# Optimization experiments

Measured on AMD Instinct MI355X. Metric: run time of the kernel, lower is better.

The kernel has to match this reference:

```python
import jax, jax.numpy as jnp
import numpy as np

IN_FEATURES = 256
OUT_FEATURES = 64
ALPHA = 0.2  # leaky relu slope


def _xavier_uniform(key, shape, gain=1.414):
    fan_in, fan_out = shape[0], shape[1]
    limit = gain * np.sqrt(6.0 / (fan_in + fan_out))
    return jax.random.uniform(key, shape, jnp.float32, -limit, limit)


def setup_inputs() -> dict:
    key = jax.random.key(0)
    k_h, k_W, k_a = jax.random.split(key, 3)
    h = jax.random.normal(k_h, (8, 2048, IN_FEATURES), dtype=jnp.float32)
    W = _xavier_uniform(k_W, (IN_FEATURES, OUT_FEATURES))
    a = _xavier_uniform(k_a, (2 * OUT_FEATURES, 1))
    return {"h": h, "W": W, "a": a}


def reference(h, W, a):
    # h: [B, N, F_in], W: [F_in, D], a: [2D, 1]
    Wh = h @ W  # [B, N, D]
    D = Wh.shape[-1]
    a1 = a[:D, 0]   # attends to source node i (repeat_interleave side)
    a2 = a[D:, 0]   # attends to target node j (repeat side)
    f1 = Wh @ a1    # [B, N]
    f2 = Wh @ a2    # [B, N]
    # e[b, i, j] = leakyrelu(a1.Wh[b,i] + a2.Wh[b,j])  -- identical math to
    # the original's O(N^2 * 2D) repeat/concat, without materializing it.
    e = jax.nn.leaky_relu(f1[:, :, None] + f2[:, None, :], negative_slope=ALPHA)  # [B, N, N]
    # NOTE: original applies softmax over dim=1 (over i, per column j).
    attention = jax.nn.softmax(e, axis=1)  # [B, N, N]
    # dropout is identity in eval mode
    h_prime = jnp.einsum('bij,bjd->bid', attention, Wh)  # [B, N, D]
    return jax.nn.elu(h_prime)  # concat=True path
```

## Files before the change

### kernel.cpp

```cpp
#include <hip/hip_runtime.h>

#define B 8
#define N 2048
#define KF 256
#define DF 64
#define LOG2E 1.44269504088896340736f
#define IC 8
#define ICH (N / IC)

typedef __attribute__((ext_vector_type(8))) short short8;
typedef __attribute__((ext_vector_type(4))) float float4v;

__device__ __forceinline__ float fexp2(float x) {
#if __has_builtin(__builtin_amdgcn_exp2f)
    return __builtin_amdgcn_exp2f(x);
#else
    return exp2f(x);
#endif
}
__device__ __forceinline__ float flog2(float x) {
#if __has_builtin(__builtin_amdgcn_logf)
    return __builtin_amdgcn_logf(x);
#else
    return log2f(x);
#endif
}
__device__ __forceinline__ float eluf(float x) {
    return x > 0.f ? x : fexp2(x * LOG2E) - 1.0f;
}
__device__ __forceinline__ short bf16r(float x) {
    unsigned u = __float_as_uint(x);
    return (short)((u + 0x8000u) >> 16);
}

__global__ __launch_bounds__(256) void k_v(const float* __restrict__ W,
                                           const float* __restrict__ a,
                                           short* __restrict__ WTg,
                                           float* __restrict__ v12) {
    int t = threadIdx.x;
    if (blockIdx.x < 64) {
        int idx = blockIdx.x * 256 + t;
        int k = idx >> 6, n = idx & 63;
        WTg[n * KF + k] = bf16r(W[idx]);
    } else {
        float s1 = 0.f, s2 = 0.f;
        for (int d = 0; d < DF; d++) {
            float w = W[t * DF + d];
            s1 = fmaf(w, a[d], s1);
            s2 = fmaf(w, a[DF + d], s2);
        }
        v12[t] = s1;
        v12[KF + t] = s2;
    }
}

__global__ __launch_bounds__(256) void k_wh(const float* __restrict__ h,
                                            const short* __restrict__ WTg,
                                            const float* __restrict__ v12,
                                            short* __restrict__ WhT,
                                            float* __restrict__ f1,
                                            float* __restrict__ f2) {
    __shared__ float lred[4 * 16 * DF];
    __shared__ float lp[2][4][16];
    int t = threadIdx.x;
    int wv = t >> 6, lane = t & 63;
    int n15 = lane & 15, q = lane >> 4;
    long i0 = (long)blockIdx.x * 16;
    const float* hr = h + (i0 + n15) * KF + wv * 64;
    const short* bp0 = WTg + n15 * KF + wv * 64;

    float4v acc0 = {0.f, 0.f, 0.f, 0.f}, acc1 = acc0, acc2 = acc0, acc3 = acc0;
    float p1 = 0.f, p2 = 0.f;

    #pragma unroll
    for (int s = 0; s < 2; s++) {
        int k0 = s * 32 + q * 8;
        int kg = wv * 64 + k0;
        float4 a0 = *(const float4*)(hr + k0);
        float4 a1 = *(const float4*)(hr + k0 + 4);
        float4 u0 = *(const float4*)(v12 + kg);
        float4 u1 = *(const float4*)(v12 + kg + 4);
        float4 x0 = *(const float4*)(v12 + KF + kg);
        float4 x1 = *(const float4*)(v12 + KF + kg + 4);
        p1 = fmaf(a0.x, u0.x, fmaf(a0.y, u0.y, fmaf(a0.z, u0.z, fmaf(a0.w, u0.w, p1))));
        p1 = fmaf(a1.x, u1.x, fmaf(a1.y, u1.y, fmaf(a1.z, u1.z, fmaf(a1.w, u1.w, p1))));
        p2 = fmaf(a0.x, x0.x, fmaf(a0.y, x0.y, fmaf(a0.z, x0.z, fmaf(a0.w, x0.w, p2))));
        p2 = fmaf(a1.x, x1.x, fmaf(a1.y, x1.y, fmaf(a1.z, x1.z, fmaf(a1.w, x1.w, p2))));

        short8 af = { bf16r(a0.x), bf16r(a0.y), bf16r(a0.z), bf16r(a0.w),
                      bf16r(a1.x), bf16r(a1.y), bf16r(a1.z), bf16r(a1.w) };
        const short* bp = bp0 + k0;
        short8 b0 = *(const short8*)(bp);
        short8 b1 = *(const short8*)(bp + 16 * KF);
        short8 b2 = *(const short8*)(bp + 32 * KF);
        short8 b3 = *(const short8*)(bp + 48 * KF);

        acc0 = __builtin_amdgcn_mfma_f32_16x16x32_bf16(af, b0, acc0, 0, 0, 0);
        acc1 = __builtin_amdgcn_mfma_f32_16x16x32_bf16(af, b1, acc1, 0, 0, 0);
        acc2 = __builtin_amdgcn_mfma_f32_16x16x32_bf16(af, b2, acc2, 0, 0, 0);
        acc3 = __builtin_amdgcn_mfma_f32_16x16x32_bf16(af, b3, acc3, 0, 0, 0);
    }

    #define STASH(nb, A)                                                 \
        {                                                                \
            _Pragma("unroll")                                            \
            for (int r = 0; r < 4; r++)                                  \
                lred[wv * 1024 + (q * 4 + r) * DF + nb * 16 + n15] = A[r]; \
        }
    STASH(0, acc0) STASH(1, acc1) STASH(2, acc2) STASH(3, acc3)
    #undef STASH

    p1 += __shfl_xor(p1, 16, 64); p1 += __shfl_xor(p1, 32, 64);
    p2 += __shfl_xor(p2, 16, 64); p2 += __shfl_xor(p2, 32, 64);
    if (q == 0) { lp[0][wv][n15] = p1; lp[1][wv][n15] = p2; }
    __syncthreads();

    int d = t & 63, ig = t >> 6;
    int bb = (int)(i0 >> 11);
    int il = (int)(i0 & (N - 1));
    float s0 = 0.f, s1 = 0.f, s2 = 0.f, s3 = 0.f;
    #pragma unroll
    for (int w = 0; w < 4; w++) {
        const float* lr = lred + w * 1024 + (ig * 4) * DF + d;
        s0 += lr[0]; s1 += lr[DF]; s2 += lr[2 * DF]; s3 += lr[3 * DF];
    }
    short4 pk = make_short4(bf16r(s0), bf16r(s1), bf16r(s2), bf16r(s3));
    int jj = il + ig * 4;
    *(short4*)(WhT + (((long)bb * 8 + (jj >> 8)) * 64 + d) * 256 + (jj & 255)) = pk;

    if (t < 16) {
        float v = lp[0][0][t] + lp[0][1][t] + lp[0][2][t] + lp[0][3][t];
        f1[i0 + t] = v;
    } else if (t < 32) {
        int tt = t - 16;
        float v = lp[1][0][tt] + lp[1][1][tt] + lp[1][2][tt] + lp[1][3][tt];
        f2[i0 + tt] = v;
    }
}

__global__ __launch_bounds__(256) void k_denom(const float* __restrict__ f1,
                                               const float* __restrict__ f2,
                                               float* __restrict__ dpart) {
    __shared__ float lf1[ICH];
    int t = threadIdx.x;
    int b = blockIdx.z, ic = blockIdx.y;
    int j = blockIdx.x * 256 + t;
    lf1[t] = f1[b * N + ic * ICH + t];
    __syncthreads();
    float f2j = f2[b * N + j];
    float s = 0.f;
    for (int ii = 0; ii < ICH; ii++) {
        float e = (lf1[ii] + f2j) * LOG2E;
        s += fexp2(fmaxf(e, 0.2f * e));
    }
    dpart[((long)ic * B + b) * N + j] = s;
}

__global__ __launch_bounds__(256) void k_attn(const short* __restrict__ WhT,
                                              const float* __restrict__ f1,
                                              const float* __restrict__ f2,
                                              const float* __restrict__ dpart,
                                              float* __restrict__ out) {
    __shared__ uint4 ls[64][33];
    __shared__ float2 lc[2][256];
    int t = threadIdx.x;
    int wv = t >> 6, lane = t & 63;
    int n15 = lane & 15, q = lane >> 4;
    int it = blockIdx.x, b = blockIdx.y;
    int i0 = it * 64 + wv * 16;

    float f1L = f1[b * N + i0 + n15] * LOG2E;
    const uint4* wsrc = (const uint4*)WhT + (long)b * 8 * 2048;
    const float* f2b = f2 + b * N;
    const float* dpb = dpart + b * N;

    uint4 r0, r1, r2, r3, r4, r5, r6, r7;
    float pf2, pd0, pd1, pd2, pd3, pd4, pd5, pd6, pd7;

    #define LOADC(cc) {                                     \
        const uint4* gp = wsrc + (cc) * 2048;               \
        r0 = gp[t];        r1 = gp[256 + t];                \
        r2 = gp[512 + t];  r3 = gp[768 + t];                \
        r4 = gp[1024 + t]; r5 = gp[1280 + t];               \
        r6 = gp[1536 + t]; r7 = gp[1792 + t];               \
    }
    #define LOADP(cc) {                                     \
        int jb = (cc) * 256 + t;                            \
        pf2 = f2b[jb];                                      \
        pd0 = dpb[jb];               pd1 = dpb[16384 + jb]; \
        pd2 = dpb[2 * 16384 + jb];   pd3 = dpb[3 * 16384 + jb]; \
        pd4 = dpb[4 * 16384 + jb];   pd5 = dpb[5 * 16384 + jb]; \
        pd6 = dpb[6 * 16384 + jb];   pd7 = dpb[7 * 16384 + jb]; \
    }
    #define STOREC() {                                      \
        int rb = t >> 5, cl = t & 31;                       \
        ls[rb][cl] = r0;      ls[8 + rb][cl] = r1;          \
        ls[16 + rb][cl] = r2; ls[24 + rb][cl] = r3;         \
        ls[32 + rb][cl] = r4; ls[40 + rb][cl] = r5;         \
        ls[48 + rb][cl] = r6; ls[56 + rb][cl] = r7;         \
    }
    #define LCC(buf) {                                      \
        float den = ((pd0 + pd1) + (pd2 + pd3)) + ((pd4 + pd5) + (pd6 + pd7)); \
        lc[buf][t] = make_float2(pf2 * LOG2E, -flog2(den)); \
    }

    LOADC(0) LOADP(0)
    STOREC() LCC(0)
    __syncthreads();

    float4v acc0 = {0.f, 0.f, 0.f, 0.f}, acc1 = acc0, acc2 = acc0, acc3 = acc0;

    for (int c = 0; c < 8; c++) {
        int cur = c & 1;
        if (c < 7) { LOADC(c + 1) LOADP(c + 1) }

        const short* lsS = (const short*)&ls[0][0];
        const float4* lcf = (const float4*)&lc[cur][0];
        #pragma unroll
        for (int js = 0; js < 8; js++) {
            const float4* cp4 = lcf + js * 16 + q * 4;
            float4 p01 = cp4[0], p23 = cp4[1], p45 = cp4[2], p67 = cp4[3];
            short8 af;
            #define PENT(F2L, LS2, DI)                        \
                {                                             \
                    float t0 = f1L + (F2L);                   \
                    float l2 = fmaxf(t0, 0.2f * t0);          \
                    af[DI] = bf16r(fexp2(l2 + (LS2)));        \
                }
            PENT(p01.x, p01.y, 0) PENT(p01.z, p01.w, 1)
            PENT(p23.x, p23.y, 2) PENT(p23.z, p23.w, 3)
            PENT(p45.x, p45.y, 4) PENT(p45.z, p45.w, 5)
            PENT(p67.x, p67.y, 6) PENT(p67.z, p67.w, 7)
            #undef PENT

            const short* bp = lsS + js * 32 + q * 8;
            short8 b0 = *(const short8*)(bp + (n15 +  0) * 264);
            short8 b1 = *(const short8*)(bp + (n15 + 16) * 264);
            short8 b2 = *(const short8*)(bp + (n15 + 32) * 264);
            short8 b3 = *(const short8*)(bp + (n15 + 48) * 264);

            acc0 = __builtin_amdgcn_mfma_f32_16x16x32_bf16(af, b0, acc0, 0, 0, 0);
            acc1 = __builtin_amdgcn_mfma_f32_16x16x32_bf16(af, b1, acc1, 0, 0, 0);
            acc2 = __builtin_amdgcn_mfma_f32_16x16x32_bf16(af, b2, acc2, 0, 0, 0);
            acc3 = __builtin_amdgcn_mfma_f32_16x16x32_bf16(af, b3, acc3, 0, 0, 0);
        }

        if (c < 7) {
            __syncthreads();
            STOREC() LCC((c + 1) & 1)
            __syncthreads();
        }
    }
    #undef LOADC
    #undef LOADP
    #undef STOREC
    #undef LCC

    float* ob = out + ((long)b * N + i0 + q * 4) * DF + n15;
    #pragma unroll
    for (int r = 0; r < 4; r++) {
        ob[r * DF + 0]  = eluf(acc0[r]);
        ob[r * DF + 16] = eluf(acc1[r]);
        ob[r * DF + 32] = eluf(acc2[r]);
        ob[r * DF + 48] = eluf(acc3[r]);
    }
}

extern "C" void kernel_launch(void* const* d_in, const int* in_sizes, int n_in,
                              void* d_out, int out_size, void* d_ws, size_t ws_size,
                              hipStream_t stream) {
    const float* h = (const float*)d_in[0];
    const float* W = (const float*)d_in[1];
    const float* a = (const float*)d_in[2];
    float* out = (float*)d_out;

    char* ws = (char*)d_ws;
    const size_t NB = (size_t)B * N;
    size_t off = 0;
    short* WTg   = (short*)(ws + off); off += (size_t)KF * DF * sizeof(short);
    float* v12   = (float*)(ws + off); off += 2 * KF * sizeof(float);
    short* WhT   = (short*)(ws + off); off += NB * DF * sizeof(short);
    float* f1    = (float*)(ws + off); off += NB * sizeof(float);
    float* f2    = (float*)(ws + off); off += NB * sizeof(float);
    float* dpart = (float*)(ws + off); off += (size_t)IC * NB * sizeof(float);
    (void)off; (void)ws_size;

    k_v<<<65, 256, 0, stream>>>(W, a, WTg, v12);
    k_wh<<<NB / 16, 256, 0, stream>>>(h, WTg, v12, WhT, f1, f2);
    k_denom<<<dim3(N / 256, IC, B), 256, 0, stream>>>(f1, f2, dpart);
    k_attn<<<dim3(N / 64, B), 256, 0, stream>>>(WhT, f1, f2, dpart, out);
}
```

Before: 105.1 us.

## Fuse all four stages into one cooperative kernel with grid syncs

Replaces four separate launches with a single cooperative kernel of 256 blocks that uses grid-wide syncs between the weight prep, Wh projection, denominator and attention stages. Each block now handles 64 rows in the projection stage and 512 i-values in the denominator stage, so the denominator partials drop from 8 to 4 chunks. This removes launch gaps and inter-kernel drain, in exchange for less parallelism per stage (256 blocks) and the cost of the grid barriers.

```diff
diff --git a/kernel.cpp b/kernel.cpp
--- a/kernel.cpp
+++ b/kernel.cpp
@@ -1,12 +1,13 @@
 #include <hip/hip_runtime.h>
+#include <hip/hip_cooperative_groups.h>
+
+namespace cg = cooperative_groups;
 
 #define B 8
 #define N 2048
 #define KF 256
 #define DF 64
 #define LOG2E 1.44269504088896340736f
-#define IC 8
-#define ICH (N / IC)
 
 typedef __attribute__((ext_vector_type(8))) short short8;
 typedef __attribute__((ext_vector_type(4))) float float4v;
@@ -32,17 +33,27 @@
     unsigned u = __float_as_uint(x);
     return (short)((u + 0x8000u) >> 16);
 }
-
-__global__ __launch_bounds__(256) void k_v(const float* __restrict__ W,
-                                           const float* __restrict__ a,
-                                           short* __restrict__ WTg,
-                                           float* __restrict__ v12) {
+#define DOT4(c, u, p) \
+    p = fmaf(c.x, u.x, fmaf(c.y, u.y, fmaf(c.z, u.z, fmaf(c.w, u.w, p))));
+
+__global__ __launch_bounds__(256) void k_mega(
+    const float* __restrict__ h, const float* __restrict__ W,
+    const float* __restrict__ a, short* __restrict__ WTg,
+    float* __restrict__ v12, short* __restrict__ WhT,
+    float* __restrict__ f1, float* __restrict__ f2,
+    float* __restrict__ dpart, float* __restrict__ out) {
+    __shared__ __align__(16) unsigned char smem[37888];
+    cg::grid_group grid = cg::this_grid();
     int t = threadIdx.x;
-    if (blockIdx.x < 64) {
-        int idx = blockIdx.x * 256 + t;
+    int bx = blockIdx.x;
+    int wv = t >> 6, lane = t & 63;
+    int n15 = lane & 15, q = lane >> 4;
+
+    if (bx < 64) {
+        int idx = bx * 256 + t;
         int k = idx >> 6, n = idx & 63;
         WTg[n * KF + k] = bf16r(W[idx]);
-    } else {
+    } else if (bx == 64) {
         float s1 = 0.f, s2 = 0.f;
         for (int d = 0; d < DF; d++) {
             float w = W[t * DF + d];
@@ -52,217 +63,219 @@
         v12[t] = s1;
         v12[KF + t] = s2;
     }
-}
-
-__global__ __launch_bounds__(256) void k_wh(const float* __restrict__ h,
-                                            const short* __restrict__ WTg,
-                                            const float* __restrict__ v12,
-                                            short* __restrict__ WhT,
-                                            float* __restrict__ f1,
-                                            float* __restrict__ f2) {
-    __shared__ float lred[4 * 16 * DF];
-    __shared__ float lp[2][4][16];
-    int t = threadIdx.x;
-    int wv = t >> 6, lane = t & 63;
-    int n15 = lane & 15, q = lane >> 4;
-    long i0 = (long)blockIdx.x * 16;
-    const float* hr = h + (i0 + n15) * KF + wv * 64;
-    const short* bp0 = WTg + n15 * KF + wv * 64;
-
-    float4v acc0 = {0.f, 0.f, 0.f, 0.f}, acc1 = acc0, acc2 = acc0, acc3 = acc0;
-    float p1 = 0.f, p2 = 0.f;
-
-    #pragma unroll
-    for (int s = 0; s < 2; s++) {
-        int k0 = s * 32 + q * 8;
-        int kg = wv * 64 + k0;
-        float4 a0 = *(const float4*)(hr + k0);
-        float4 a1 = *(const float4*)(hr + k0 + 4);
-        float4 u0 = *(const float4*)(v12 + kg);
-        float4 u1 = *(const float4*)(v12 + kg + 4);
-        float4 x0 = *(const float4*)(v12 + KF + kg);
-        float4 x1 = *(const float4*)(v12 + KF + kg + 4);
-        p1 = fmaf(a0.x, u0.x, fmaf(a0.y, u0.y, fmaf(a0.z, u0.z, fmaf(a0.w, u0.w, p1))));
-        p1 = fmaf(a1.x, u1.x, fmaf(a1.y, u1.y, fmaf(a1.z, u1.z, fmaf(a1.w, u1.w, p1))));
-        p2 = fmaf(a0.x, x0.x, fmaf(a0.y, x0.y, fmaf(a0.z, x0.z, fmaf(a0.w, x0.w, p2))));
-        p2 = fmaf(a1.x, x1.x, fmaf(a1.y, x1.y, fmaf(a1.z, x1.z, fmaf(a1.w, x1.w, p2))));
-
-        short8 af = { bf16r(a0.x), bf16r(a0.y), bf16r(a0.z), bf16r(a0.w),
-                      bf16r(a1.x), bf16r(a1.y), bf16r(a1.z), bf16r(a1.w) };
-        const short* bp = bp0 + k0;
-        short8 b0 = *(const short8*)(bp);
-        short8 b1 = *(const short8*)(bp + 16 * KF);
-        short8 b2 = *(const short8*)(bp + 32 * KF);
-        short8 b3 = *(const short8*)(bp + 48 * KF);
-
-        acc0 = __builtin_amdgcn_mfma_f32_16x16x32_bf16(af, b0, acc0, 0, 0, 0);
-        acc1 = __builtin_amdgcn_mfma_f32_16x16x32_bf16(af, b1, acc1, 0, 0, 0);
-        acc2 = __builtin_amdgcn_mfma_f32_16x16x32_bf16(af, b2, acc2, 0, 0, 0);
-        acc3 = __builtin_amdgcn_mfma_f32_16x16x32_bf16(af, b3, acc3, 0, 0, 0);
+    grid.sync();
+
+    {
+        float* lred = (float*)smem;
+        float* lp = (float*)(smem + 16384);
+        const short* bq = WTg + n15 * KF + wv * 64 + q * 8;
+        short8 s0b0 = *(const short8*)(bq);
+        short8 s0b1 = *(const short8*)(bq + 16 * KF);
+        short8 s0b2 = *(const short8*)(bq + 32 * KF);
+        short8 s0b3 = *(const short8*)(bq + 48 * KF);
+        short8 s1b0 = *(const short8*)(bq + 32);
+        short8 s1b1 = *(const short8*)(bq + 16 * KF + 32);
+        short8 s1b2 = *(const short8*)(bq + 32 * KF + 32);
+        short8 s1b3 = *(const short8*)(bq + 48 * KF + 32);
+        const float* vv = v12 + wv * 64 + q * 8;
+        float4 u00 = *(const float4*)(vv);
+        float4 u01 = *(const float4*)(vv + 4);
+        float4 u10 = *(const float4*)(vv + 32);
+        float4 u11 = *(const float4*)(vv + 36);
+        float4 x00 = *(const float4*)(vv + KF);
+        float4 x01 = *(const float4*)(vv + KF + 4);
+        float4 x10 = *(const float4*)(vv + KF + 32);
+        float4 x11 = *(const float4*)(vv + KF + 36);
+
+        const float* hr = h + ((long)bx * 64 + n15) * KF + wv * 64 + q * 8;
+        float4 c0 = *(const float4*)(hr);
+        float4 c1 = *(const float4*)(hr + 4);
+        float4 c2 = *(const float4*)(hr + 32);
+        float4 c3 = *(const float4*)(hr + 36);
+
+        #pragma unroll
+        for (int rt = 0; rt < 4; rt++) {
+            float4 m0, m1, m2, m3;
+            if (rt < 3) {
+                const float* hn = hr + (rt + 1) * 16 * KF;
+                m0 = *(const float4*)(hn);
+                m1 = *(const float4*)(hn + 4);
+                m2 = *(const float4*)(hn + 32);
+                m3 = *(const float4*)(hn + 36);
+            }
+            float p1 = 0.f, p2 = 0.f;
+            DOT4(c0, u00, p1) DOT4(c1, u01, p1) DOT4(c2, u10, p1) DOT4(c3, u11, p1)
+            DOT4(c0, x00, p2) DOT4(c1, x01, p2) DOT4(c2, x10, p2) DOT4(c3, x11, p2)
+
+            short8 af0 = { bf16r(c0.x), bf16r(c0.y), bf16r(c0.z), bf16r(c0.w),
+                           bf16r(c1.x), bf16r(c1.y), bf16r(c1.z), bf16r(c1.w) };
+            short8 af1 = { bf16r(c2.x), bf16r(c2.y), bf16r(c2.z), bf16r(c2.w),
+                           bf16r(c3.x), bf16r(c3.y), bf16r(c3.z), bf16r(c3.w) };
+            float4v acc0 = {0.f, 0.f, 0.f, 0.f}, acc1 = acc0, acc2 = acc0, acc3 = acc0;
+            acc0 = __builtin_amdgcn_mfma_f32_16x16x32_bf16(af0, s0b0, acc0, 0, 0, 0);
+            acc0 = __builtin_amdgcn_mfma_f32_16x16x32_bf16(af1, s1b0, acc0, 0, 0, 0);
+            acc1 = __builtin_amdgcn_mfma_f32_16x16x32_bf16(af0, s0b1, acc1, 0, 0, 0);
+            acc1 = __builtin_amdgcn_mfma_f32_16x16x32_bf16(af1, s1b1, acc1, 0, 0, 0);
+            acc2 = __builtin_amdgcn_mfma_f32_16x16x32_bf16(af0, s0b2, acc2, 0, 0, 0);
+            acc2 = __builtin_amdgcn_mfma_f32_16x16x32_bf16(af1, s1b2, acc2, 0, 0, 0);
+            acc3 = __builtin_amdgcn_mfma_f32_16x16x32_bf16(af0, s0b3, acc3, 0, 0, 0);
+            acc3 = __builtin_amdgcn_mfma_f32_16x16x32_bf16(af1, s1b3, acc3, 0, 0, 0);
+
+            #define STASH(nb, A)                                                 \
+                {                                                                \
+                    _Pragma("unroll")                                            \
+                    for (int r = 0; r < 4; r++)                                  \
+                        lred[wv * 1024 + (q * 4 + r) * DF + nb * 16 + n15] = A[r]; \
+                }
+            STASH(0, acc0) STASH(1, acc1) STASH(2, acc2) STASH(3, acc3)
+            #undef STASH
+            p1 += __shfl_xor(p1, 16, 64); p1 += __shfl_xor(p1, 32, 64);
+            p2 += __shfl_xor(p2, 16, 64); p2 += __shfl_xor(p2, 32, 64);
+            if (q == 0) { lp[wv * 16 + n15] = p1; lp[64 + wv * 16 + n15] = p2; }
+            __syncthreads();
+
+            long i0 = (long)bx * 64 + rt * 16;
+            int d = t & 63, ig = t >> 6;
+            int bb = (int)(i0 >> 11);
+            int il = (int)(i0 & (N - 1));
+            float s0 = 0.f, s1 = 0.f, s2 = 0.f, s3 = 0.f;
+            #pragma unroll
+            for (int w = 0; w < 4; w++) {
+                const float* lr = lred + w * 1024 + (ig * 4) * DF + d;
+                s0 += lr[0]; s1 += lr[DF]; s2 += lr[2 * DF]; s3 += lr[3 * DF];
+            }
+            short4 pk = make_short4(bf16r(s0), bf16r(s1), bf16r(s2), bf16r(s3));
+            int jj = il + ig * 4;
+            *(short4*)(WhT + (((long)bb * 8 + (jj >> 8)) * 64 + d) * 256 + (jj & 255)) = pk;
+
+            if (t < 16) {
+                f1[i0 + t] = lp[t] + lp[16 + t] + lp[32 + t] + lp[48 + t];
+            } else if (t < 32) {
+                int tt = t + 48;
+                f2[i0 + t - 16] = lp[tt] + lp[16 + tt] + lp[32 + tt] + lp[48 + tt];
+            }
+            __syncthreads();
+            c0 = m0; c1 = m1; c2 = m2; c3 = m3;
+        }
     }
-
-    #define STASH(nb, A)                                                 \
-        {                                                                \
-            _Pragma("unroll")                                            \
-            for (int r = 0; r < 4; r++)                                  \
-                lred[wv * 1024 + (q * 4 + r) * DF + nb * 16 + n15] = A[r]; \
-        }
-    STASH(0, acc0) STASH(1, acc1) STASH(2, acc2) STASH(3, acc3)
-    #undef STASH
-
-    p1 += __shfl_xor(p1, 16, 64); p1 += __shfl_xor(p1, 32, 64);
-    p2 += __shfl_xor(p2, 16, 64); p2 += __shfl_xor(p2, 32, 64);
-    if (q == 0) { lp[0][wv][n15] = p1; lp[1][wv][n15] = p2; }
-    __syncthreads();
-
-    int d = t & 63, ig = t >> 6;
-    int bb = (int)(i0 >> 11);
-    int il = (int)(i0 & (N - 1));
-    float s0 = 0.f, s1 = 0.f, s2 = 0.f, s3 = 0.f;
-    #pragma unroll
-    for (int w = 0; w < 4; w++) {
-        const float* lr = lred + w * 1024 + (ig * 4) * DF + d;
-        s0 += lr[0]; s1 += lr[DF]; s2 += lr[2 * DF]; s3 += lr[3 * DF];
+    grid.sync();
+
+    {
+        float* lf1 = (float*)smem;
+        int jb = bx & 7, ic = (bx >> 3) & 3, b2 = bx >> 5;
+        lf1[t] = f1[b2 * N + ic * 512 + t];
+        lf1[256 + t] = f1[b2 * N + ic * 512 + 256 + t];
+        __syncthreads();
+        float f2j = f2[b2 * N + jb * 256 + t];
+        float s = 0.f;
+        for (int ii = 0; ii < 512; ii++) {
+            float e = (lf1[ii] + f2j) * LOG2E;
+            s += fexp2(fmaxf(e, 0.2f * e));
+        }
+        dpart[((long)ic * B + b2) * N + jb * 256 + t] = s;
+        __syncthreads();
     }
-    short4 pk = make_short4(bf16r(s0), bf16r(s1), bf16r(s2), bf16r(s3));
-    int jj = il + ig * 4;
-    *(short4*)(WhT + (((long)bb * 8 + (jj >> 8)) * 64 + d) * 256 + (jj & 255)) = pk;
-
-    if (t < 16) {
-        float v = lp[0][0][t] + lp[0][1][t] + lp[0][2][t] + lp[0][3][t];
-        f1[i0 + t] = v;
-    } else if (t < 32) {
-        int tt = t - 16;
-        float v = lp[1][0][tt] + lp[1][1][tt] + lp[1][2][tt] + lp[1][3][tt];
-        f2[i0 + tt] = v;
-    }
-}
-
-__global__ __launch_bounds__(256) void k_denom(const float* __restrict__ f1,
-                                               const float* __restrict__ f2,
-                                               float* __restrict__ dpart) {
-    __shared__ float lf1[ICH];
-    int t = threadIdx.x;
-    int b = blockIdx.z, ic = blockIdx.y;
-    int j = blockIdx.x * 256 + t;
-    lf1[t] = f1[b * N + ic * ICH + t];
-    __syncthreads();
-    float f2j = f2[b * N + j];
-    float s = 0.f;
-    for (int ii = 0; ii < ICH; ii++) {
-        float e = (lf1[ii] + f2j) * LOG2E;
-        s += fexp2(fmaxf(e, 0.2f * e));
-    }
-    dpart[((long)ic * B + b) * N + j] = s;
-}
-
-__global__ __launch_bounds__(256) void k_attn(const short* __restrict__ WhT,
-                                              const float* __restrict__ f1,
-                                              const float* __restrict__ f2,
-                                              const float* __restrict__ dpart,
-                                              float* __restrict__ out) {
-    __shared__ uint4 ls[64][33];
-    __shared__ float2 lc[2][256];
-    int t = threadIdx.x;
-    int wv = t >> 6, lane = t & 63;
-    int n15 = lane & 15, q = lane >> 4;
-    int it = blockIdx.x, b = blockIdx.y;
-    int i0 = it * 64 + wv * 16;
-
-    float f1L = f1[b * N + i0 + n15] * LOG2E;
-    const uint4* wsrc = (const uint4*)WhT + (long)b * 8 * 2048;
-    const float* f2b = f2 + b * N;
-    const float* dpb = dpart + b * N;
-
-    uint4 r0, r1, r2, r3, r4, r5, r6, r7;
-    float pf2, pd0, pd1, pd2, pd3, pd4, pd5, pd6, pd7;
-
-    #define LOADC(cc) {                                     \
-        const uint4* gp = wsrc + (cc) * 2048;               \
-        r0 = gp[t];        r1 = gp[256 + t];                \
-        r2 = gp[512 + t];  r3 = gp[768 + t];                \
-        r4 = gp[1024 + t]; r5 = gp[1280 + t];               \
-        r6 = gp[1536 + t]; r7 = gp[1792 + t];               \
-    }
-    #define LOADP(cc) {                                     \
-        int jb = (cc) * 256 + t;                            \
-        pf2 = f2b[jb];                                      \
-        pd0 = dpb[jb];               pd1 = dpb[16384 + jb]; \
-        pd2 = dpb[2 * 16384 + jb];   pd3 = dpb[3 * 16384 + jb]; \
-        pd4 = dpb[4 * 16384 + jb];   pd5 = dpb[5 * 16384 + jb]; \
-        pd6 = dpb[6 * 16384 + jb];   pd7 = dpb[7 * 16384 + jb]; \
-    }
-    #define STOREC() {                                      \
-        int rb = t >> 5, cl = t & 31;                       \
-        ls[rb][cl] = r0;      ls[8 + rb][cl] = r1;          \
-        ls[16 + rb][cl] = r2; ls[24 + rb][cl] = r3;         \
-        ls[32 + rb][cl] = r4; ls[40 + rb][cl] = r5;         \
-        ls[48 + rb][cl] = r6; ls[56 + rb][cl] = r7;         \
-    }
-    #define LCC(buf) {                                      \
-        float den = ((pd0 + pd1) + (pd2 + pd3)) + ((pd4 + pd5) + (pd6 + pd7)); \
-        lc[buf][t] = make_float2(pf2 * LOG2E, -flog2(den)); \
-    }
-
-    LOADC(0) LOADP(0)
-    STOREC() LCC(0)
-    __syncthreads();
-
-    float4v acc0 = {0.f, 0.f, 0.f, 0.f}, acc1 = acc0, acc2 = acc0, acc3 = acc0;
-
-    for (int c = 0; c < 8; c++) {
-        int cur = c & 1;
-        if (c < 7) { LOADC(c + 1) LOADP(c + 1) }
-
-        const short* lsS = (const short*)&ls[0][0];
-        const float4* lcf = (const float4*)&lc[cur][0];
+    grid.sync();
+
+    {
+        uint4 (*ls)[33] = (uint4 (*)[33])smem;
+        float2 (*lc)[256] = (float2 (*)[256])(smem + 33792);
+        int it = bx & 31, b3 = bx >> 5;
+        int i0 = it * 64 + wv * 16;
+
+        float f1L = f1[b3 * N + i0 + n15] * LOG2E;
+        const uint4* wsrc = (const uint4*)WhT + (long)b3 * 8 * 2048;
+        const float* f2b = f2 + b3 * N;
+        const float* dpb = dpart + b3 * N;
+
+        uint4 r0, r1, r2, r3, r4, r5, r6, r7;
+        float pf2, pd0, pd1, pd2, pd3;
+
+        #define LOADC(cc) {                                     \
+            const uint4* gp = wsrc + (cc) * 2048;               \
+            r0 = gp[t];        r1 = gp[256 + t];                \
+            r2 = gp[512 + t];  r3 = gp[768 + t];                \
+            r4 = gp[1024 + t]; r5 = gp[1280 + t];               \
+            r6 = gp[1536 + t]; r7 = gp[1792 + t];               \
+        }
+        #define LOADP(cc) {                                     \
+            int jb2 = (cc) * 256 + t;                           \
+            pf2 = f2b[jb2];                                     \
+            pd0 = dpb[jb2];              pd1 = dpb[16384 + jb2];\
+            pd2 = dpb[2 * 16384 + jb2];  pd3 = dpb[3 * 16384 + jb2]; \
+        }
+        #define STOREC() {                                      \
+            int rb = t >> 5, cl = t & 31;                       \
+            ls[rb][cl] = r0;      ls[8 + rb][cl] = r1;          \
+            ls[16 + rb][cl] = r2; ls[24 + rb][cl] = r3;         \
+            ls[32 + rb][cl] = r4; ls[40 + rb][cl] = r5;         \
+            ls[48 + rb][cl] = r6; ls[56 + rb][cl] = r7;         \
+        }
+        #define LCC(buf) {                                      \
+            float den = (pd0 + pd1) + (pd2 + pd3);              \
+            lc[buf][t] = make_float2(pf2 * LOG2E, -flog2(den)); \
+        }
+
+        LOADC(0) LOADP(0)
+        STOREC() LCC(0)
+        __syncthreads();
+
+        float4v acc0 = {0.f, 0.f, 0.f, 0.f}, acc1 = acc0, acc2 = acc0, acc3 = acc0;
+
+        for (int c = 0; c < 8; c++) {
+            int cur = c & 1;
+            if (c < 7) { LOADC(c + 1) LOADP(c + 1) }
+
+            const short* lsS = (const short*)smem;
+            const float4* lcf = (const float4*)&lc[cur][0];
+            #pragma unroll
+            for (int js = 0; js < 8; js++) {
+                const float4* cp4 = lcf + js * 16 + q * 4;
+                float4 p01 = cp4[0], p23 = cp4[1], p45 = cp4[2], p67 = cp4[3];
+                short8 af;
+                #define PENT(F2L, LS2, DI)                        \
+                    {                                             \
+                        float t0 = f1L + (F2L);                   \
+                        float l2 = fmaxf(t0, 0.2f * t0);          \
+                        af[DI] = bf16r(fexp2(l2 + (LS2)));        \
+                    }
+                PENT(p01.x, p01.y, 0) PENT(p01.z, p01.w, 1)
+                PENT(p23.x, p23.y, 2) PENT(p23.z, p23.w, 3)
+                PENT(p45.x, p45.y, 4) PENT(p45.z, p45.w, 5)
+                PENT(p67.x, p67.y, 6) PENT(p67.z, p67.w, 7)
+                #undef PENT
+
+                const short* bp = lsS + js * 32 + q * 8;
+                short8 b0 = *(const short8*)(bp + (n15 +  0) * 264);
+                short8 b1 = *(const short8*)(bp + (n15 + 16) * 264);
+                short8 b2 = *(const short8*)(bp + (n15 + 32) * 264);
+                short8 b3 = *(const short8*)(bp + (n15 + 48) * 264);
+
+                acc0 = __builtin_amdgcn_mfma_f32_16x16x32_bf16(af, b0, acc0, 0, 0, 0);
+                acc1 = __builtin_amdgcn_mfma_f32_16x16x32_bf16(af, b1, acc1, 0, 0, 0);
+                acc2 = __builtin_amdgcn_mfma_f32_16x16x32_bf16(af, b2, acc2, 0, 0, 0);
+                acc3 = __builtin_amdgcn_mfma_f32_16x16x32_bf16(af, b3, acc3, 0, 0, 0);
+            }
+
+            if (c < 7) {
+                __syncthreads();
+                STOREC() LCC((c + 1) & 1)
+                __syncthreads();
+            }
+        }
+        #undef LOADC
+        #undef LOADP
+        #undef STOREC
+        #undef LCC
+
+        float* ob = out + ((long)b3 * N + i0 + q * 4) * DF + n15;
         #pragma unroll
-        for (int js = 0; js < 8; js++) {
-            const float4* cp4 = lcf + js * 16 + q * 4;
-            float4 p01 = cp4[0], p23 = cp4[1], p45 = cp4[2], p67 = cp4[3];
-            short8 af;
-            #define PENT(F2L, LS2, DI)                        \
-                {                                             \
-                    float t0 = f1L + (F2L);                   \
-                    float l2 = fmaxf(t0, 0.2f * t0);          \
-                    af[DI] = bf16r(fexp2(l2 + (LS2)));        \
-                }
-            PENT(p01.x, p01.y, 0) PENT(p01.z, p01.w, 1)
-            PENT(p23.x, p23.y, 2) PENT(p23.z, p23.w, 3)
-            PENT(p45.x, p45.y, 4) PENT(p45.z, p45.w, 5)
-            PENT(p67.x, p67.y, 6) PENT(p67.z, p67.w, 7)
-            #undef PENT
-
-            const short* bp = lsS + js * 32 + q * 8;
-            short8 b0 = *(const short8*)(bp + (n15 +  0) * 264);
-            short8 b1 = *(const short8*)(bp + (n15 + 16) * 264);
-            short8 b2 = *(const short8*)(bp + (n15 + 32) * 264);
-            short8 b3 = *(const short8*)(bp + (n15 + 48) * 264);
-
-            acc0 = __builtin_amdgcn_mfma_f32_16x16x32_bf16(af, b0, acc0, 0, 0, 0);
-            acc1 = __builtin_amdgcn_mfma_f32_16x16x32_bf16(af, b1, acc1, 0, 0, 0);
-            acc2 = __builtin_amdgcn_mfma_f32_16x16x32_bf16(af, b2, acc2, 0, 0, 0);
-            acc3 = __builtin_amdgcn_mfma_f32_16x16x32_bf16(af, b3, acc3, 0, 0, 0);
-        }
-
-        if (c < 7) {
-            __syncthreads();
-            STOREC() LCC((c + 1) & 1)
-            __syncthreads();
-        }
-    }
-    #undef LOADC
-    #undef LOADP
-    #undef STOREC
-    #undef LCC
-
-    float* ob = out + ((long)b * N + i0 + q * 4) * DF + n15;
-    #pragma unroll
-    for (int r = 0; r < 4; r++) {
-        ob[r * DF + 0]  = eluf(acc0[r]);
-        ob[r * DF + 16] = eluf(acc1[r]);
-        ob[r * DF + 32] = eluf(acc2[r]);
-        ob[r * DF + 48] = eluf(acc3[r]);
+        for (int r = 0; r < 4; r++) {
+            ob[r * DF + 0]  = eluf(acc0[r]);
+            ob[r * DF + 16] = eluf(acc1[r]);
+            ob[r * DF + 32] = eluf(acc2[r]);
+            ob[r * DF + 48] = eluf(acc3[r]);
+        }
     }
 }
 
@@ -282,11 +295,10 @@
     short* WhT   = (short*)(ws + off); off += NB * DF * sizeof(short);
     float* f1    = (float*)(ws + off); off += NB * sizeof(float);
     float* f2    = (float*)(ws + off); off += NB * sizeof(float);
-    float* dpart = (float*)(ws + off); off += (size_t)IC * NB * sizeof(float);
+    float* dpart = (float*)(ws + off); off += 4 * NB * sizeof(float);
     (void)off; (void)ws_size;
 
-    k_v<<<65, 256, 0, stream>>>(W, a, WTg, v12);
-    k_wh<<<NB / 16, 256, 0, stream>>>(h, WTg, v12, WhT, f1, f2);
-    k_denom<<<dim3(N / 256, IC, B), 256, 0, stream>>>(f1, f2, dpart);
-    k_attn<<<dim3(N / 64, B), 256, 0, stream>>>(WhT, f1, f2, dpart, out);
-}
+    void* args[] = {(void*)&h, (void*)&W, (void*)&a, (void*)&WTg, (void*)&v12,
+                    (void*)&WhT, (void*)&f1, (void*)&f2, (void*)&dpart, (void*)&out};
+    hipLaunchCooperativeKernel((void*)k_mega, dim3(256), dim3(256), args, 0, stream);
+}
```

Result: slower. 196.8 us (+87.2%).
